# Optimization experiments

Hardware: AMD Instinct MI355X
Metric: run time of the kernel (lower is better)

Reference implementation:

```python
import jax, jax.numpy as jnp
import numpy as np

# --- constants from cfg (dmc.__init__) ---
DT = 3600.0            # self.t
P_SPATIAL = 21.0       # cfg.params.defaults.p
VEL_LB, VEL_UB = 0.3, 15.0
DEPTH_LB = 0.01
Q_LB = 1e-4            # discharge lower bound
BW_LB = 0.1            # bottom width lower bound
SLOPE_MIN = 1e-4
N_LO, N_HI = 0.01, 0.35          # Manning n bounds (denormalize)
QS_LO, QS_HI = 0.0, 3.0          # q_spatial bounds

# --- river network: perfect binary confluence tree, topologically ordered ---
LEVELS = 17
SIZES = [2 ** (LEVELS - 1 - l) for l in range(LEVELS)]   # 65536 leaves ... 1 outlet
OFFS = np.concatenate([[0], np.cumsum(SIZES)]).astype(np.int64)
N_NODES = int(OFFS[-1])  # 131071; internal nodes are indices OFFS[1]..N_NODES-1 (contiguous)


def _tree_edges():
    src, dst, cl, cr = [], [], [], []
    for l in range(1, LEVELS):
        k = np.arange(SIZES[l], dtype=np.int64)
        p = OFFS[l] + k
        c0 = OFFS[l - 1] + 2 * k
        c1 = OFFS[l - 1] + 2 * k + 1
        src += [c0, c1]
        dst += [p, p]
        cl.append(c0)
        cr.append(c1)
    return (np.concatenate(src).astype(np.int32), np.concatenate(dst).astype(np.int32),
            np.concatenate(cl).astype(np.int32), np.concatenate(cr).astype(np.int32))


def setup_inputs() -> dict:
    T = 336
    key = jax.random.key(0)
    ks = jax.random.split(key, 8)
    u = lambda k, s: jax.random.uniform(k, s, dtype=jnp.float32)
    q_prime = 0.1 + 5.0 * u(ks[0], (T, N_NODES))          # lateral inflow, m^3/s
    n_raw = u(ks[1], (N_NODES,))
    q_spatial_raw = u(ks[2], (N_NODES,))
    length = 500.0 + 4500.0 * u(ks[3], (N_NODES,))        # reach length, m
    slope = 1e-4 + 0.05 * u(ks[4], (N_NODES,))            # channel slope
    top_width = 2.0 + 48.0 * u(ks[5], (N_NODES,))         # m
    side_slope = 0.5 + 1.5 * u(ks[6], (N_NODES,))
    x_storage = 0.3 * u(ks[7], (N_NODES,))                # Muskingum x
    es, ed, cl, cr = _tree_edges()
    return {"q_prime": q_prime, "n_raw": n_raw, "q_spatial_raw": q_spatial_raw,
            "length": length, "slope": slope, "top_width": top_width,
            "side_slope": side_slope, "x_storage": x_storage,
            "edge_src": jnp.asarray(es), "edge_dst": jnp.asarray(ed),
            "child_left": jnp.asarray(cl), "child_right": jnp.asarray(cr)}


def _velocity(q_t, n, q_spatial, top_width, side_slope, s0):
    """_get_trapezoid_velocity: Manning's equation on a trapezoidal channel."""
    num = q_t * n * (q_spatial + 1.0)
    den = P_SPATIAL * jnp.sqrt(s0)
    depth = jnp.maximum(jnp.power(num / (den + 1e-8), 3.0 / (5.0 + 3.0 * q_spatial)), DEPTH_LB)
    bottom = jnp.maximum(top_width - 2.0 * side_slope * depth, BW_LB)
    area = (top_width + bottom) * depth * 0.5
    wetted = bottom + 2.0 * depth * jnp.sqrt(1.0 + side_slope ** 2)
    R = area / wetted
    v = (1.0 / n) * jnp.power(R, 2.0 / 3.0) * jnp.sqrt(s0)
    return jnp.clip(v, VEL_LB, VEL_UB) * (5.0 / 3.0)


def _routing(q_prime, n, qs, length, s0, top_width, side_slope, x,
             edge_src, edge_dst, child_left, child_right):
    nn = q_prime.shape[1]
    # static level scheduling for the lower-triangular solve
    parent_idx = [jnp.asarray(OFFS[l] + np.arange(SIZES[l]), dtype=jnp.int32) for l in range(1, LEVELS)]
    lvl_bounds = [(int(OFFS[l] - OFFS[1]), int(OFFS[l + 1] - OFFS[1])) for l in range(1, LEVELS)]

    def step(q, qp_prev):
        qpc = jnp.maximum(qp_prev, Q_LB)
        v = _velocity(q, n, qs, top_width, side_slope, s0)
        k = length / v
        denom = 2.0 * k * (1.0 - x) + DT
        c2 = (DT + 2.0 * k * x) / denom
        c3 = (2.0 * k * (1.0 - x) - DT) / denom
        c4 = 2.0 * DT / denom
        c1 = (DT - 2.0 * k * x) / denom
        c1_ = (-c1).at[0].set(1.0)                     # as in original (row 0 is a headwater)
        i_t = jax.ops.segment_sum(q[edge_src], edge_dst, num_segments=nn)  # N @ q
        b = c2 * i_t + c3 * q + c4 * qpc
        # solve (I + diag(c1_) N) q1 = b by forward substitution, level by level
        q1 = b                                          # leaves: q1 = b
        for li in range(LEVELS - 1):
            p = parent_idx[li]
            s, e = lvl_bounds[li]
            cl, cr = child_left[s:e], child_right[s:e]
            q1 = q1.at[p].set(b[p] - c1_[p] * (q1[cl] + q1[cr]))
        q1 = jnp.maximum(q1, Q_LB)
        return q1, q1[-1]                               # outlet gage (gage_idx = -1)

    q0 = q_prime[0]                                     # initial discharge state
    _, ys = jax.lax.scan(step, q0, q_prime[:-1])        # timesteps 1..T-1 use q_prime[t-1]
    out0 = jnp.maximum(q_prime[0, -1], Q_LB)
    return jnp.concatenate([out0[None], ys])[None, :]   # [1, T] runoff at gage


def reference(q_prime, n_raw, q_spatial_raw, length, slope, top_width, side_slope,
              x_storage, edge_src, edge_dst, child_left, child_right):
    n = N_LO + n_raw * (N_HI - N_LO)                    # denormalize
    qs = QS_LO + q_spatial_raw * (QS_HI - QS_LO)
    s0 = jnp.maximum(slope, SLOPE_MIN)
    return _routing(q_prime, n, qs, length, s0, top_width, side_slope, x_storage,
                    edge_src, edge_dst, child_left, child_right)
```

## Files before the change

### kernel.cpp

```cpp
#include <hip/hip_runtime.h>

#define Q_LBF 1e-4f
#define DTF   3600.0f
#define NN    131071
#define SENT  0x7FC00001u
#define W1    2048
#define W2    32
#define PRESYNC_ROW 20

#if __has_builtin(__builtin_amdgcn_exp2f)
#define FEXP2(x) __builtin_amdgcn_exp2f(x)
#else
#define FEXP2(x) exp2f(x)
#endif
#if __has_builtin(__builtin_amdgcn_logf)
#define FLOG2(x) __builtin_amdgcn_logf(x)
#else
#define FLOG2(x) log2f(x)
#endif
#if __has_builtin(__builtin_amdgcn_rcpf)
#define FRCP(x) __builtin_amdgcn_rcpf(x)
#else
#define FRCP(x) (1.0f/(x))
#endif

struct NC { float a1, e, tw, ssd, w2, a2, kd, kx; };

__device__ __forceinline__ NC make_nc(const float* __restrict__ nr,
                                      const float* __restrict__ qsr,
                                      const float* __restrict__ len,
                                      const float* __restrict__ slp,
                                      const float* __restrict__ twp,
                                      const float* __restrict__ ssp,
                                      const float* __restrict__ xsp,
                                      int g) {
  float n  = fmaf(nr[g], 0.34f, 0.01f);
  float qs = 3.0f * qsr[g];
  float s0 = fmaxf(slp[g], 1e-4f);
  float rs = sqrtf(s0);
  float L  = len[g];
  float x  = xsp[g];
  float ss = ssp[g];
  NC c;
  c.a1  = n * (qs + 1.0f) / fmaf(21.0f, rs, 1e-8f);
  c.e   = 3.0f / fmaf(3.0f, qs, 5.0f);
  c.tw  = twp[g];
  c.ssd = 2.0f * ss;
  c.w2  = 2.0f * sqrtf(fmaf(ss, ss, 1.0f));
  c.a2  = rs / n;
  float kl = 1.2f * L;
  c.kd  = kl * (1.0f - x);
  c.kx  = kl * x;
  return c;
}

__device__ __forceinline__ float node_b(const NC& c, float q, float qpc, float it,
                                        float& c1o) {
  float z    = q * c.a1;
  float d    = fmaxf(FEXP2(c.e * FLOG2(z)), 0.01f);
  float bot  = fmaxf(fmaf(-c.ssd, d, c.tw), 0.1f);
  float area = (c.tw + bot) * (0.5f * d);
  float wet  = fmaf(c.w2, d, bot);
  float R    = area * FRCP(wet);
  float v2   = c.a2 * FEXP2(0.66666668f * FLOG2(R));
  v2 = fminf(fmaxf(v2, 0.3f), 15.0f);
  float rv   = FRCP(v2);
  float rden = FRCP(fmaf(c.kd, rv, DTF));
  float c2   = fmaf(c.kx, rv, DTF) * rden;
  float c4   = 7200.0f * rden;
  c1o = c4 - c2;
  float c3 = 1.0f - c4;
  return fmaf(c2, it, fmaf(c3, q, c4 * qpc));
}

__device__ __forceinline__ int iclamp(int v, int lo, int hi) {
  return v < lo ? lo : (v > hi ? hi : v);
}

__device__ __forceinline__ void st_stream(float* p, float v) {
  __hip_atomic_store((unsigned*)p, __float_as_uint(v),
                     __ATOMIC_RELAXED, __HIP_MEMORY_SCOPE_AGENT);
}
__device__ __forceinline__ uint2 ld2_relaxed(const float* p) {
  const unsigned* u = (const unsigned*)p;
  uint2 r;
  r.x = __hip_atomic_load(u,     __ATOMIC_RELAXED, __HIP_MEMORY_SCOPE_AGENT);
  r.y = __hip_atomic_load(u + 1, __ATOMIC_RELAXED, __HIP_MEMORY_SCOPE_AGENT);
  return r;
}
__device__ __forceinline__ uint2 ld2_block(const float* p) {
  uint2 r = ld2_relaxed(p);
  while (r.x == SENT || r.y == SENT) {
    __builtin_amdgcn_s_sleep(1);
    r = ld2_relaxed(p);
  }
  return r;
}
__device__ __forceinline__ uint2 ld2_plain(const float* p) {
  return *reinterpret_cast<const uint2*>(p);
}

__device__ __forceinline__ void run_A(
    const float* __restrict__ qp,
    const float* __restrict__ nr, const float* __restrict__ qsr,
    const float* __restrict__ len, const float* __restrict__ slp,
    const float* __restrict__ twp, const float* __restrict__ ssp,
    const float* __restrict__ xsp,
    float* __restrict__ S1, float* __restrict__ D1, int w, int lane) {
  int e, g, cs0;
  const bool leaf = lane < 32;
  if (leaf)           { e = 0; g = (w << 5) + lane;               cs0 = 0; }
  else if (lane < 48) { e = 1; g = 65536  + (w << 4) + (lane-32); cs0 = 2*(lane-32); }
  else if (lane < 56) { e = 2; g = 98304  + (w << 3) + (lane-48); cs0 = 32 + 2*(lane-48); }
  else if (lane < 60) { e = 3; g = 114688 + (w << 2) + (lane-56); cs0 = 48 + 2*(lane-56); }
  else if (lane < 62) { e = 4; g = 122880 + (w << 1) + (lane-60); cs0 = 56 + 2*(lane-60); }
  else                { e = 5; g = 126976 + w;                    cs0 = 60; }
  NC c = make_nc(nr,qsr,len,slp,twp,ssp,xsp, g);
  float q0 = qp[g];
  float i0 = __shfl(q0, cs0), i1 = __shfl(q0, cs0 + 1);
  const float itInit = i0 + i1;
  if (lane == 62) st_stream(&S1[w], q0);
  float qc = q0, ul = q0, pu0 = 0.0f, pu1 = 0.0f;
  float rg[8];
#pragma unroll
  for (int j = 0; j < 8; ++j) rg[j] = qp[iclamp(j - e, 0, 335) * NN + g];
  int off = (8 - e) * NN + g;
  const int offMax = 335 * NN + g;
  for (int so = 0; so < 344; so += 8) {
#pragma unroll
    for (int j = 0; j < 8; ++j) {
      const int s = so + j;
      float u0 = __shfl(ul, cs0), u1 = __shfl(ul, cs0 + 1);
      float itg = (s == e) ? itInit : (fmaxf(pu0, Q_LBF) + fmaxf(pu1, Q_LBF));
      if (s == e) qc = q0;
      float it  = leaf ? 0.0f : itg;
      float chn = leaf ? 0.0f : (u0 + u1);
      float qpc = fmaxf(rg[j], Q_LBF);
      float c1;
      float b  = node_b(c, qc, qpc, it, c1);
      float un = fmaf(c1, chn, b);
      qc = fmaxf(un, Q_LBF); ul = un;
      pu0 = u0; pu1 = u1;
      float* dst = (s >= 5 && s <= 339) ? (S1 + (s - 4) * W1 + w) : (D1 + w);
      if (lane == 62) st_stream(dst, un);
      rg[j] = qp[off];
      off = min(off + NN, offMax);
    }
  }
}

__device__ __forceinline__ void run_B(
    const float* __restrict__ qp,
    const float* __restrict__ nr, const float* __restrict__ qsr,
    const float* __restrict__ len, const float* __restrict__ slp,
    const float* __restrict__ twp, const float* __restrict__ ssp,
    const float* __restrict__ xsp,
    const float* __restrict__ S1, float* __restrict__ S2,
    float* __restrict__ D2, int r, int lane) {
  int e, g, cs0;
  const bool leaf = lane < 32;
  const int jl = leaf ? lane : 31;
  if (leaf)           { e = 0; g = 129024 + (r << 5) + lane;      cs0 = 0; }
  else if (lane < 48) { e = 1; g = 130048 + (r << 4) + (lane-32); cs0 = 2*(lane-32); }
  else if (lane < 56) { e = 2; g = 130560 + (r << 3) + (lane-48); cs0 = 32 + 2*(lane-48); }
  else if (lane < 60) { e = 3; g = 130816 + (r << 2) + (lane-56); cs0 = 48 + 2*(lane-56); }
  else if (lane < 62) { e = 4; g = 130944 + (r << 1) + (lane-60); cs0 = 56 + 2*(lane-60); }
  else                { e = 5; g = 131008 + r;                    cs0 = 60; }
  const int col2 = ((r << 5) + jl) * 2;
  NC c = make_nc(nr,qsr,len,slp,twp,ssp,xsp, g);
  float q0 = qp[g];
  float i0 = __shfl(q0, cs0), i1 = __shfl(q0, cs0 + 1);
  const float itInit = i0 + i1;
  if (lane == 62) st_stream(&S2[r], q0);
  {
    uint2 t0 = ld2_block(S1 + PRESYNC_ROW * W1 + col2);
    asm volatile("" :: "v"(t0.x), "v"(t0.y));
  }
  float qc = q0, ul = q0, pu0 = 0.0f, pu1 = 0.0f;
  uint2 rgs[8];
  float rg[8];
#pragma unroll
  for (int j = 0; j < 8; ++j) rgs[j] = ld2_plain(S1 + iclamp(j, 0, 335) * W1 + col2);
#pragma unroll
  for (int j = 0; j < 8; ++j) rg[j] = qp[iclamp(j - e, 0, 335) * NN + g];
  int off = (8 - e) * NN + g;
  const int offMax = 335 * NN + g;
  int soff = 8 * W1 + col2;
  const int soffMax = 335 * W1 + col2;
  __builtin_amdgcn_s_setprio(2);
  for (int so = 0; so < 344; so += 8) {
#pragma unroll
    for (int j = 0; j < 8; ++j) {
      const int s = so + j;
      uint2 fo = rgs[j];
      uint2 fn = rgs[(j + 1) & 7];
      if (__builtin_expect((fo.x == SENT) | (fo.y == SENT) |
                           (fn.x == SENT) | (fn.y == SENT), 0)) {
        __builtin_amdgcn_s_setprio(0);
        fo = ld2_block(S1 + iclamp(s,     0, 335) * W1 + col2);
        fn = ld2_block(S1 + iclamp(s + 1, 0, 335) * W1 + col2);
        __builtin_amdgcn_s_setprio(2);
        rgs[(j + 1) & 7] = fn;
      }
      float fox = __uint_as_float(fo.x), foy = __uint_as_float(fo.y);
      float fnx = __uint_as_float(fn.x), fny = __uint_as_float(fn.y);
      float u0 = __shfl(ul, cs0), u1 = __shfl(ul, cs0 + 1);
      float itg = (s == e) ? itInit : (fmaxf(pu0, Q_LBF) + fmaxf(pu1, Q_LBF));
      if (s == e) qc = q0;
      float it  = leaf ? (fmaxf(fox, Q_LBF) + fmaxf(foy, Q_LBF)) : itg;
      float chn = leaf ? (fnx + fny) : (u0 + u1);
      float qpc = fmaxf(rg[j], Q_LBF);
      float c1;
      float b  = node_b(c, qc, qpc, it, c1);
      float un = fmaf(c1, chn, b);
      qc = fmaxf(un, Q_LBF); ul = un;
      pu0 = u0; pu1 = u1;
      float* dst = (s >= 5 && s <= 339) ? (S2 + (s - 4) * W2 + r) : (D2 + r);
      if (lane == 62) st_stream(dst, un);
      rgs[j] = ld2_plain(S1 + soff);
      rg[j]  = qp[off];
      off  = min(off + NN, offMax);
      soff = min(soff + W1, soffMax);
    }
  }
  __builtin_amdgcn_s_setprio(0);
}

__device__ __forceinline__ void run_C(
    const float* __restrict__ qp,
    const float* __restrict__ nr, const float* __restrict__ qsr,
    const float* __restrict__ len, const float* __restrict__ slp,
    const float* __restrict__ twp, const float* __restrict__ ssp,
    const float* __restrict__ xsp,
    const float* __restrict__ S2, float* __restrict__ out, int lane) {
  int e, g, cs0;
  const bool leaf = lane < 16;
  const int jl = leaf ? lane : 15;
  if (leaf)           { e = 0; g = 131040 + lane;        cs0 = 0; }
  else if (lane < 24) { e = 1; g = 131056 + (lane - 16); cs0 = 2*(lane-16); }
  else if (lane < 28) { e = 2; g = 131064 + (lane - 24); cs0 = 16 + 2*(lane-24); }
  else if (lane < 30) { e = 3; g = 131068 + (lane - 28); cs0 = 24 + 2*(lane-28); }
  else                { e = 4; g = 131070;               cs0 = 28; }
  const int col2 = jl * 2;
  NC c = make_nc(nr,qsr,len,slp,twp,ssp,xsp, g);
  float q0 = qp[g];
  float i0 = __shfl(q0, cs0), i1 = __shfl(q0, cs0 + 1);
  const float itInit = i0 + i1;
  if (lane == 30) out[0] = fmaxf(q0, Q_LBF);
  {
    uint2 t0 = ld2_block(S2 + PRESYNC_ROW * W2 + col2);
    asm volatile("" :: "v"(t0.x), "v"(t0.y));
  }
  float qc = q0, ul = q0, pu0 = 0.0f, pu1 = 0.0f;
  uint2 rgs[8];
  float rg[8];
#pragma unroll
  for (int j = 0; j < 8; ++j) rgs[j] = ld2_plain(S2 + iclamp(j, 0, 335) * W2 + col2);
#pragma unroll
  for (int j = 0; j < 8; ++j) rg[j] = qp[iclamp(j - e, 0, 335) * NN + g];
  int off = (8 - e) * NN + g;
  const int offMax = 335 * NN + g;
  int soff = 8 * W2 + col2;
  const int soffMax = 335 * W2 + col2;
  __builtin_amdgcn_s_setprio(3);
  for (int so = 0; so < 344; so += 8) {
#pragma unroll
    for (int j = 0; j < 8; ++j) {
      const int s = so + j;
      uint2 fo = rgs[j];
      uint2 fn = rgs[(j + 1) & 7];
      if (__builtin_expect((fo.x == SENT) | (fo.y == SENT) |
                           (fn.x == SENT) | (fn.y == SENT), 0)) {
        __builtin_amdgcn_s_setprio(0);
        fo = ld2_block(S2 + iclamp(s,     0, 335) * W2 + col2);
        fn = ld2_block(S2 + iclamp(s + 1, 0, 335) * W2 + col2);
        __builtin_amdgcn_s_setprio(3);
        rgs[(j + 1) & 7] = fn;
      }
      float fox = __uint_as_float(fo.x), foy = __uint_as_float(fo.y);
      float fnx = __uint_as_float(fn.x), fny = __uint_as_float(fn.y);
      float u0 = __shfl(ul, cs0), u1 = __shfl(ul, cs0 + 1);
      float itg = (s == e) ? itInit : (fmaxf(pu0, Q_LBF) + fmaxf(pu1, Q_LBF));
      if (s == e) qc = q0;
      float it  = leaf ? (fmaxf(fox, Q_LBF) + fmaxf(foy, Q_LBF)) : itg;
      float chn = leaf ? (fnx + fny) : (u0 + u1);
      float qpc = fmaxf(rg[j], Q_LBF);
      float c1;
      float b  = node_b(c, qc, qpc, it, c1);
      float un = fmaf(c1, chn, b);
      qc = fmaxf(un, Q_LBF); ul = un;
      pu0 = u0; pu1 = u1;
      if (lane == 30 && s >= 4 && s <= 338) out[s - 3] = fmaxf(un, Q_LBF);
      rgs[j] = ld2_plain(S2 + soff);
      rg[j]  = qp[off];
      off  = min(off + NN, offMax);
      soff = min(soff + W2, soffMax);
    }
  }
  __builtin_amdgcn_s_setprio(0);
}

__global__ __launch_bounds__(256) void kinit(unsigned* __restrict__ F, int n) {
  int i = blockIdx.x * 256 + threadIdx.x;
  int stride = gridDim.x * 256;
  for (; i < n; i += stride) F[i] = SENT;
}

__global__ __launch_bounds__(576, 3) void fused(
    const float* __restrict__ qp,
    const float* __restrict__ nr, const float* __restrict__ qsr,
    const float* __restrict__ len, const float* __restrict__ slp,
    const float* __restrict__ twp, const float* __restrict__ ssp,
    const float* __restrict__ xsp,
    float* __restrict__ S1, float* __restrict__ S2,
    float* __restrict__ D1, float* __restrict__ D2,
    float* __restrict__ out) {
  const int wv = threadIdx.x >> 6;
  const int lane = threadIdx.x & 63;
  const int b = blockIdx.x;
  if (wv < 8) {
    run_A(qp, nr, qsr, len, slp, twp, ssp, xsp, S1, D1, (b << 3) + wv, lane);
  } else if (b < 32) {
    run_B(qp, nr, qsr, len, slp, twp, ssp, xsp, S1, S2, D2, b, lane);
  } else if (b == 32) {
    run_C(qp, nr, qsr, len, slp, twp, ssp, xsp, S2, out, lane);
  }
}

extern "C" void kernel_launch(void* const* d_in, const int* in_sizes, int n_in,
                              void* d_out, int out_size, void* d_ws, size_t ws_size,
                              hipStream_t stream) {
  const float* q_prime = (const float*)d_in[0];
  const float* n_raw   = (const float*)d_in[1];
  const float* qs_raw  = (const float*)d_in[2];
  const float* length  = (const float*)d_in[3];
  const float* slope   = (const float*)d_in[4];
  const float* tw      = (const float*)d_in[5];
  const float* ss      = (const float*)d_in[6];
  const float* xs      = (const float*)d_in[7];
  float* out = (float*)d_out;
  float* S1 = (float*)d_ws;
  float* S2 = S1 + 336 * W1;
  float* D1 = S2 + 336 * W2;
  float* D2 = D1 + W1;
  const int nsent = 336 * W1 + 336 * W2 + W1 + W2;
  kinit<<<128, 256, 0, stream>>>((unsigned*)d_ws, nsent);
  fused<<<256, 576, 0, stream>>>(q_prime, n_raw, qs_raw, length, slope, tw, ss, xs,
                                 S1, S2, D1, D2, out);
}
```

Baseline: 329.6 us.

## Stream per-step inputs through LDS with global_load_lds and explicit vmcnt waits

The register ring buffers for q_prime and upstream stage values are replaced by direct global-to-LDS loads (global_load_lds), with manual s_waitcnt vmcnt counts and sched barriers. Every lane now issues a store each step, and non-writer lanes target a dump slot, so the outstanding-memory counter stays uniform and the fixed vmcnt thresholds hold. The aim is to take the loads off the latency-critical serial recurrence and cut VGPR pressure. The risk is that hand-tuned vmcnt counts are fragile, and the extra dummy stores add memory traffic.

```diff
diff --git a/kernel.cpp b/kernel.cpp
--- a/kernel.cpp
+++ b/kernel.cpp
@@ -23,6 +23,14 @@
 #else
 #define FRCP(x) (1.0f/(x))
 #endif
+
+#define SBAR() __builtin_amdgcn_sched_barrier(0)
+
+__device__ __forceinline__ void gload4(const float* g, float* l) {
+  __builtin_amdgcn_global_load_lds(
+      (const __attribute__((address_space(1))) unsigned*)g,
+      (__attribute__((address_space(3))) unsigned*)l, 4, 0, 0);
+}
 
 struct NC { float a1, e, tw, ssd, w2, a2, kd, kx; };
 
@@ -96,9 +104,6 @@
   }
   return r;
 }
-__device__ __forceinline__ uint2 ld2_plain(const float* p) {
-  return *reinterpret_cast<const uint2*>(p);
-}
 
 __device__ __forceinline__ void run_A(
     const float* __restrict__ qp,
@@ -106,7 +111,8 @@
     const float* __restrict__ len, const float* __restrict__ slp,
     const float* __restrict__ twp, const float* __restrict__ ssp,
     const float* __restrict__ xsp,
-    float* __restrict__ S1, float* __restrict__ D1, int w, int lane) {
+    float* __restrict__ S1, float* __restrict__ D1,
+    float* lds, int w, int lane) {
   int e, g, cs0;
   const bool leaf = lane < 32;
   if (leaf)           { e = 0; g = (w << 5) + lane;               cs0 = 0; }
@@ -120,31 +126,41 @@
   float i0 = __shfl(q0, cs0), i1 = __shfl(q0, cs0 + 1);
   const float itInit = i0 + i1;
   if (lane == 62) st_stream(&S1[w], q0);
+  float* dumpP = D1 + w;
+  const int offMax = 335 * NN + g;
+#pragma unroll
+  for (int j = 0; j < 8; ++j) {
+    st_stream(dumpP, 0.0f);
+    gload4(qp + iclamp(j - e, 0, 335) * NN + g, lds + j * 64);
+    SBAR();
+  }
+  int off = (8 - e) * NN + g;
+  asm volatile("s_waitcnt vmcnt(0)" ::: "memory"); SBAR();
+  float Q = lds[lane];
   float qc = q0, ul = q0, pu0 = 0.0f, pu1 = 0.0f;
-  float rg[8];
-#pragma unroll
-  for (int j = 0; j < 8; ++j) rg[j] = qp[iclamp(j - e, 0, 335) * NN + g];
-  int off = (8 - e) * NN + g;
-  const int offMax = 335 * NN + g;
   for (int so = 0; so < 344; so += 8) {
 #pragma unroll
     for (int j = 0; j < 8; ++j) {
       const int s = so + j;
+      asm volatile("s_waitcnt vmcnt(10)" ::: "memory"); SBAR();
+      float Qn = lds[((j + 1) & 7) * 64 + lane];
       float u0 = __shfl(ul, cs0), u1 = __shfl(ul, cs0 + 1);
       float itg = (s == e) ? itInit : (fmaxf(pu0, Q_LBF) + fmaxf(pu1, Q_LBF));
       if (s == e) qc = q0;
       float it  = leaf ? 0.0f : itg;
       float chn = leaf ? 0.0f : (u0 + u1);
-      float qpc = fmaxf(rg[j], Q_LBF);
+      float qpc = fmaxf(Q, Q_LBF);
       float c1;
       float b  = node_b(c, qc, qpc, it, c1);
       float un = fmaf(c1, chn, b);
       qc = fmaxf(un, Q_LBF); ul = un;
       pu0 = u0; pu1 = u1;
-      float* dst = (s >= 5 && s <= 339) ? (S1 + (s - 4) * W1 + w) : (D1 + w);
-      if (lane == 62) st_stream(dst, un);
-      rg[j] = qp[off];
+      float* dst = (lane == 62 && s >= 5 && s <= 339) ? (S1 + (s - 4) * W1 + w)
+                                                      : dumpP;
+      st_stream(dst, un);
+      gload4(qp + off, lds + j * 64);
       off = min(off + NN, offMax);
+      Q = Qn;
     }
   }
 }
@@ -156,7 +172,7 @@
     const float* __restrict__ twp, const float* __restrict__ ssp,
     const float* __restrict__ xsp,
     const float* __restrict__ S1, float* __restrict__ S2,
-    float* __restrict__ D2, int r, int lane) {
+    float* __restrict__ D2, float* lds, int r, int lane) {
   int e, g, cs0;
   const bool leaf = lane < 32;
   const int jl = leaf ? lane : 31;
@@ -176,51 +192,65 @@
     uint2 t0 = ld2_block(S1 + PRESYNC_ROW * W1 + col2);
     asm volatile("" :: "v"(t0.x), "v"(t0.y));
   }
+  SBAR();
+  float* dumpP = D2 + r;
+  const int offMax  = 335 * NN + g;
+  const int soffMax = 335 * W1 + col2;
+#pragma unroll
+  for (int j = 0; j < 8; ++j) {
+    st_stream(dumpP, 0.0f);
+    gload4(S1 + j * W1 + col2,     lds + j * 192);
+    gload4(S1 + j * W1 + col2 + 1, lds + j * 192 + 64);
+    gload4(qp + iclamp(j - e, 0, 335) * NN + g, lds + j * 192 + 128);
+    SBAR();
+  }
+  int soff = 8 * W1 + col2;
+  int off  = (8 - e) * NN + g;
+  asm volatile("s_waitcnt vmcnt(0)" ::: "memory"); SBAR();
+  float r0x = lds[lane],       r0y = lds[64 + lane];
+  float r1x = lds[192 + lane], r1y = lds[192 + 64 + lane];
+  float Q   = lds[128 + lane];
   float qc = q0, ul = q0, pu0 = 0.0f, pu1 = 0.0f;
-  uint2 rgs[8];
-  float rg[8];
-#pragma unroll
-  for (int j = 0; j < 8; ++j) rgs[j] = ld2_plain(S1 + iclamp(j, 0, 335) * W1 + col2);
-#pragma unroll
-  for (int j = 0; j < 8; ++j) rg[j] = qp[iclamp(j - e, 0, 335) * NN + g];
-  int off = (8 - e) * NN + g;
-  const int offMax = 335 * NN + g;
-  int soff = 8 * W1 + col2;
-  const int soffMax = 335 * W1 + col2;
   __builtin_amdgcn_s_setprio(2);
   for (int so = 0; so < 344; so += 8) {
 #pragma unroll
     for (int j = 0; j < 8; ++j) {
       const int s = so + j;
-      uint2 fo = rgs[j];
-      uint2 fn = rgs[(j + 1) & 7];
-      if (__builtin_expect((fo.x == SENT) | (fo.y == SENT) |
-                           (fn.x == SENT) | (fn.y == SENT), 0)) {
+      asm volatile("s_waitcnt vmcnt(18)" ::: "memory"); SBAR();
+      float n2x = lds[((j + 2) & 7) * 192 + lane];
+      float n2y = lds[((j + 2) & 7) * 192 + 64 + lane];
+      float Qn  = lds[((j + 1) & 7) * 192 + 128 + lane];
+      if (__builtin_expect((__float_as_uint(r0x) == SENT) |
+                           (__float_as_uint(r0y) == SENT) |
+                           (__float_as_uint(r1x) == SENT) |
+                           (__float_as_uint(r1y) == SENT), 0)) {
         __builtin_amdgcn_s_setprio(0);
-        fo = ld2_block(S1 + iclamp(s,     0, 335) * W1 + col2);
-        fn = ld2_block(S1 + iclamp(s + 1, 0, 335) * W1 + col2);
+        uint2 fo = ld2_block(S1 + iclamp(s,     0, 335) * W1 + col2);
+        uint2 fn = ld2_block(S1 + iclamp(s + 1, 0, 335) * W1 + col2);
         __builtin_amdgcn_s_setprio(2);
-        rgs[(j + 1) & 7] = fn;
+        r0x = __uint_as_float(fo.x); r0y = __uint_as_float(fo.y);
+        r1x = __uint_as_float(fn.x); r1y = __uint_as_float(fn.y);
       }
-      float fox = __uint_as_float(fo.x), foy = __uint_as_float(fo.y);
-      float fnx = __uint_as_float(fn.x), fny = __uint_as_float(fn.y);
       float u0 = __shfl(ul, cs0), u1 = __shfl(ul, cs0 + 1);
       float itg = (s == e) ? itInit : (fmaxf(pu0, Q_LBF) + fmaxf(pu1, Q_LBF));
       if (s == e) qc = q0;
-      float it  = leaf ? (fmaxf(fox, Q_LBF) + fmaxf(foy, Q_LBF)) : itg;
-      float chn = leaf ? (fnx + fny) : (u0 + u1);
-      float qpc = fmaxf(rg[j], Q_LBF);
+      float it  = leaf ? (fmaxf(r0x, Q_LBF) + fmaxf(r0y, Q_LBF)) : itg;
+      float chn = leaf ? (r1x + r1y) : (u0 + u1);
+      float qpc = fmaxf(Q, Q_LBF);
       float c1;
       float b  = node_b(c, qc, qpc, it, c1);
       float un = fmaf(c1, chn, b);
       qc = fmaxf(un, Q_LBF); ul = un;
       pu0 = u0; pu1 = u1;
-      float* dst = (s >= 5 && s <= 339) ? (S2 + (s - 4) * W2 + r) : (D2 + r);
-      if (lane == 62) st_stream(dst, un);
-      rgs[j] = ld2_plain(S1 + soff);
-      rg[j]  = qp[off];
+      float* dst = (lane == 62 && s >= 5 && s <= 339) ? (S2 + (s - 4) * W2 + r)
+                                                      : dumpP;
+      st_stream(dst, un);
+      gload4(S1 + soff,     lds + j * 192);
+      gload4(S1 + soff + 1, lds + j * 192 + 64);
+      gload4(qp + off,      lds + j * 192 + 128);
+      soff = min(soff + W1, soffMax);
       off  = min(off + NN, offMax);
-      soff = min(soff + W1, soffMax);
+      r0x = r1x; r0y = r1y; r1x = n2x; r1y = n2y; Q = Qn;
     }
   }
   __builtin_amdgcn_s_setprio(0);
@@ -232,7 +262,8 @@
     const float* __restrict__ len, const float* __restrict__ slp,
     const float* __restrict__ twp, const float* __restrict__ ssp,
     const float* __restrict__ xsp,
-    const float* __restrict__ S2, float* __restrict__ out, int lane) {
+    const float* __restrict__ S2, float* __restrict__ D2,
+    float* __restrict__ out, float* lds, int lane) {
   int e, g, cs0;
   const bool leaf = lane < 16;
   const int jl = leaf ? lane : 15;
@@ -251,50 +282,64 @@
     uint2 t0 = ld2_block(S2 + PRESYNC_ROW * W2 + col2);
     asm volatile("" :: "v"(t0.x), "v"(t0.y));
   }
+  SBAR();
+  float* dumpP = D2 + 32;
+  const int offMax  = 335 * NN + g;
+  const int soffMax = 335 * W2 + col2;
+#pragma unroll
+  for (int j = 0; j < 8; ++j) {
+    st_stream(dumpP, 0.0f);
+    gload4(S2 + j * W2 + col2,     lds + j * 192);
+    gload4(S2 + j * W2 + col2 + 1, lds + j * 192 + 64);
+    gload4(qp + iclamp(j - e, 0, 335) * NN + g, lds + j * 192 + 128);
+    SBAR();
+  }
+  int soff = 8 * W2 + col2;
+  int off  = (8 - e) * NN + g;
+  asm volatile("s_waitcnt vmcnt(0)" ::: "memory"); SBAR();
+  float r0x = lds[lane],       r0y = lds[64 + lane];
+  float r1x = lds[192 + lane], r1y = lds[192 + 64 + lane];
+  float Q   = lds[128 + lane];
   float qc = q0, ul = q0, pu0 = 0.0f, pu1 = 0.0f;
-  uint2 rgs[8];
-  float rg[8];
-#pragma unroll
-  for (int j = 0; j < 8; ++j) rgs[j] = ld2_plain(S2 + iclamp(j, 0, 335) * W2 + col2);
-#pragma unroll
-  for (int j = 0; j < 8; ++j) rg[j] = qp[iclamp(j - e, 0, 335) * NN + g];
-  int off = (8 - e) * NN + g;
-  const int offMax = 335 * NN + g;
-  int soff = 8 * W2 + col2;
-  const int soffMax = 335 * W2 + col2;
   __builtin_amdgcn_s_setprio(3);
   for (int so = 0; so < 344; so += 8) {
 #pragma unroll
     for (int j = 0; j < 8; ++j) {
       const int s = so + j;
-      uint2 fo = rgs[j];
-      uint2 fn = rgs[(j + 1) & 7];
-      if (__builtin_expect((fo.x == SENT) | (fo.y == SENT) |
-                           (fn.x == SENT) | (fn.y == SENT), 0)) {
+      asm volatile("s_waitcnt vmcnt(18)" ::: "memory"); SBAR();
+      float n2x = lds[((j + 2) & 7) * 192 + lane];
+      float n2y = lds[((j + 2) & 7) * 192 + 64 + lane];
+      float Qn  = lds[((j + 1) & 7) * 192 + 128 + lane];
+      if (__builtin_expect((__float_as_uint(r0x) == SENT) |
+                           (__float_as_uint(r0y) == SENT) |
+                           (__float_as_uint(r1x) == SENT) |
+                           (__float_as_uint(r1y) == SENT), 0)) {
         __builtin_amdgcn_s_setprio(0);
-        fo = ld2_block(S2 + iclamp(s,     0, 335) * W2 + col2);
-        fn = ld2_block(S2 + iclamp(s + 1, 0, 335) * W2 + col2);
+        uint2 fo = ld2_block(S2 + iclamp(s,     0, 335) * W2 + col2);
+        uint2 fn = ld2_block(S2 + iclamp(s + 1, 0, 335) * W2 + col2);
         __builtin_amdgcn_s_setprio(3);
-        rgs[(j + 1) & 7] = fn;
+        r0x = __uint_as_float(fo.x); r0y = __uint_as_float(fo.y);
+        r1x = __uint_as_float(fn.x); r1y = __uint_as_float(fn.y);
       }
-      float fox = __uint_as_float(fo.x), foy = __uint_as_float(fo.y);
-      float fnx = __uint_as_float(fn.x), fny = __uint_as_float(fn.y);
       float u0 = __shfl(ul, cs0), u1 = __shfl(ul, cs0 + 1);
       float itg = (s == e) ? itInit : (fmaxf(pu0, Q_LBF) + fmaxf(pu1, Q_LBF));
       if (s == e) qc = q0;
-      float it  = leaf ? (fmaxf(fox, Q_LBF) + fmaxf(foy, Q_LBF)) : itg;
-      float chn = leaf ? (fnx + fny) : (u0 + u1);
-      float qpc = fmaxf(rg[j], Q_LBF);
+      float it  = leaf ? (fmaxf(r0x, Q_LBF) + fmaxf(r0y, Q_LBF)) : itg;
+      float chn = leaf ? (r1x + r1y) : (u0 + u1);
+      float qpc = fmaxf(Q, Q_LBF);
       float c1;
       float b  = node_b(c, qc, qpc, it, c1);
       float un = fmaf(c1, chn, b);
       qc = fmaxf(un, Q_LBF); ul = un;
       pu0 = u0; pu1 = u1;
-      if (lane == 30 && s >= 4 && s <= 338) out[s - 3] = fmaxf(un, Q_LBF);
-      rgs[j] = ld2_plain(S2 + soff);
-      rg[j]  = qp[off];
+      float* dst = (lane == 30 && s >= 4 && s <= 338) ? (out + (s - 3)) : dumpP;
+      st_stream(dst, fmaxf(un, Q_LBF));
+      gload4(S2 + soff,     lds + j * 192);
+      gload4(S2 + soff + 1, lds + j * 192 + 64);
+      gload4(qp + off,      lds + j * 192 + 128);
+      soff = min(soff + W2, soffMax);
       off  = min(off + NN, offMax);
-      soff = min(soff + W2, soffMax);
+      r0x = r1x; r0y = r1y; r1x = n2x; r1y = n2y; Q = Qn;
     }
   }
   __builtin_amdgcn_s_setprio(0);
@@ -315,15 +360,19 @@
     float* __restrict__ S1, float* __restrict__ S2,
     float* __restrict__ D1, float* __restrict__ D2,
     float* __restrict__ out) {
+  __shared__ float pool[8 * 512 + 8 * 192];
   const int wv = threadIdx.x >> 6;
   const int lane = threadIdx.x & 63;
   const int b = blockIdx.x;
   if (wv < 8) {
-    run_A(qp, nr, qsr, len, slp, twp, ssp, xsp, S1, D1, (b << 3) + wv, lane);
+    run_A(qp, nr, qsr, len, slp, twp, ssp, xsp, S1, D1,
+          pool + wv * 512, (b << 3) + wv, lane);
   } else if (b < 32) {
-    run_B(qp, nr, qsr, len, slp, twp, ssp, xsp, S1, S2, D2, b, lane);
+    run_B(qp, nr, qsr, len, slp, twp, ssp, xsp, S1, S2, D2,
+          pool + 4096, b, lane);
   } else if (b == 32) {
-    run_C(qp, nr, qsr, len, slp, twp, ssp, xsp, S2, out, lane);
+    run_C(qp, nr, qsr, len, slp, twp, ssp, xsp, S2, D2, out,
+          pool + 4096, lane);
   }
 }
 
@@ -343,7 +392,7 @@
   float* S2 = S1 + 336 * W1;
   float* D1 = S2 + 336 * W2;
   float* D2 = D1 + W1;
-  const int nsent = 336 * W1 + 336 * W2 + W1 + W2;
+  const int nsent = 336 * W1 + 336 * W2;
   kinit<<<128, 256, 0, stream>>>((unsigned*)d_ws, nsent);
   fused<<<256, 576, 0, stream>>>(q_prime, n_raw, qs_raw, length, slope, tw, ss, xs,
                                  S1, S2, D1, D2, out);
```

Result: slower. 525.3 us (+59.4%).
